# Kernel tuning notes

Hardware: AMD Instinct MI355X
Metric: run time of the kernel (lower is better)

## Reference

```python
import jax, jax.numpy as jnp
import numpy as np

B, S, D, H, DFF, L = 16, 1024, 64, 4, 256, 2
DEPTH = D // H
C1, C2, NOUT = 64, 64, 1
EPS = 1e-6


def setup_inputs() -> dict:
    key = jax.random.key(0)
    ks = jax.random.split(key, 24)
    s = 0.02
    vals = jax.random.normal(ks[0], (B, S), jnp.float32)
    nanp = jax.random.uniform(ks[1], (B, S)) < 0.1
    inputs = jnp.where(nanp, jnp.nan, vals)
    inp = {
        'inputs': inputs,
        'embedding': jax.random.normal(ks[2], (S, D - 1), jnp.float32) * s,
        'wq': jax.random.normal(ks[3], (L, D, D), jnp.float32) * s,
        'wq_b': jnp.zeros((L, D), jnp.float32),
        'wk': jax.random.normal(ks[4], (L, D, D), jnp.float32) * s,
        'wk_b': jnp.zeros((L, D), jnp.float32),
        'wv': jax.random.normal(ks[5], (L, D, D), jnp.float32) * s,
        'wv_b': jnp.zeros((L, D), jnp.float32),
        'wo': jax.random.normal(ks[6], (L, D, D), jnp.float32) * s,
        'ffn_w1': jax.random.normal(ks[7], (L, D, DFF), jnp.float32) * s,
        'ffn_w2': jax.random.normal(ks[8], (L, DFF, D), jnp.float32) * s,
        'ln1_g': jnp.ones((L, D), jnp.float32),
        'ln1_b': jnp.zeros((L, D), jnp.float32),
        'ln2_g': jnp.ones((L, D), jnp.float32),
        'ln2_b': jnp.zeros((L, D), jnp.float32),
        'c_w1': jax.random.normal(ks[9], (D, C1), jnp.float32) * s,
        'c_b1': jnp.zeros((C1,), jnp.float32),
        'c_w2': jax.random.normal(ks[10], (C1, C2), jnp.float32) * s,
        'c_b2': jnp.zeros((C2,), jnp.float32),
        'c_w3': jax.random.normal(ks[11], (C2, NOUT), jnp.float32) * s,
        'c_b3': jnp.zeros((NOUT,), jnp.float32),
        'out_bias': jax.random.normal(ks[12], (1, NOUT), jnp.float32),
    }
    return inp


def _layer_norm(x, g, b):
    m = jnp.mean(x, axis=-1, keepdims=True)
    v = jnp.mean((x - m) ** 2, axis=-1, keepdims=True)
    return (x - m) / jnp.sqrt(v + EPS) * g + b


def _forward(inputs, embedding, wq, wq_b, wk, wk_b, wv, wv_b, wo,
             ffn_w1, ffn_w2, ln1_g, ln1_b, ln2_g, ln2_b,
             c_w1, c_b1, c_w2, c_b2, c_w3, c_b3, out_bias):
    nan_mask = jnp.isnan(inputs)                           # (B,S) bool
    x_in = jnp.where(nan_mask, jnp.zeros_like(inputs), inputs)
    # mask (B,1,S,S): masked if either attribute i or j is NaN
    mask = (nan_mask[:, :, None] | nan_mask[:, None, :]).astype(jnp.float32)[:, None, :, :]
    # keep factor: zeros out NaN attribute rows after each sub-block  (B,S,1)
    keep = 1.0 - jnp.transpose(jnp.prod(mask, axis=-1), (0, 2, 1))

    # positional/attribute embedding: table * sqrt(d-1) * sqrt(d)
    attr = embedding * jnp.sqrt(jnp.float32(D - 1)) * jnp.sqrt(jnp.float32(D))  # (S, D-1)
    attr = jnp.broadcast_to(attr[None], (B, S, D - 1))
    x = jnp.concatenate([attr, x_in[:, :, None]], axis=2)  # (B,S,D)
    x = x * keep

    scale = 1.0 / jnp.sqrt(jnp.float32(DEPTH))
    for i in range(L):
        q = (x @ wq[i] + wq_b[i]).reshape(B, S, H, DEPTH).transpose(0, 2, 1, 3)
        k = (x @ wk[i] + wk_b[i]).reshape(B, S, H, DEPTH).transpose(0, 2, 1, 3)
        v = (x @ wv[i] + wv_b[i]).reshape(B, S, H, DEPTH).transpose(0, 2, 1, 3)
        logits = jnp.einsum('bhqd,bhkd->bhqk', q, k) * scale + mask * (-1e9)
        attn = jax.nn.softmax(logits, axis=-1) * (1.0 - mask)  # post-softmax multiplicative mask
        ctx = jnp.einsum('bhqk,bhkd->bhqd', attn, v)
        ctx = ctx.transpose(0, 2, 1, 3).reshape(B, S, D) @ wo[i]
        out1 = _layer_norm(x + ctx, ln1_g[i], ln1_b[i]) * keep
        ffn = jax.nn.relu(out1 @ ffn_w1[i]) @ ffn_w2[i]
        x = _layer_norm(out1 + ffn, ln2_g[i], ln2_b[i]) * keep

    h = jax.nn.relu(x @ c_w1 + c_b1)
    h = jax.nn.relu(h @ c_w2 + c_b2)
    phi = h @ c_w3 + c_b3                                   # (B,S,NOUT)
    y = jnp.sum(phi, axis=1) + out_bias                     # (B,NOUT)
    return y


def reference(inputs, embedding, wq, wq_b, wk, wk_b, wv, wv_b, wo,
              ffn_w1, ffn_w2, ln1_g, ln1_b, ln2_g, ln2_b,
              c_w1, c_b1, c_w2, c_b2, c_w3, c_b3, out_bias):
    return _forward(inputs, embedding, wq, wq_b, wk, wk_b, wv, wv_b, wo,
                    ffn_w1, ffn_w2, ln1_g, ln1_b, ln2_g, ln2_b,
                    c_w1, c_b1, c_w2, c_b2, c_w3, c_b3, out_bias)
```

## Files before the change

### kernel.cpp

```cpp
#include <hip/hip_runtime.h>
#include <hip/hip_bf16.h>
#include <math.h>

#define BB 16
#define SS 1024
#define DD 64
#define HH 4
#define DEPTH 16
#define DFF 256
#define NROWS (BB*SS)
#define EPSV 1e-6f
#define NKSPLIT 8
#define KCHUNK (SS / NKSPLIT)

__device__ __forceinline__ float bcast(float x, int kk) {
  return __int_as_float(__builtin_amdgcn_readlane(__float_as_int(x), kk));
}

__global__ __launch_bounds__(256) void build_x_kernel(
    const float* __restrict__ inputs, const float* __restrict__ emb,
    float* __restrict__ x, float* __restrict__ keep) {
  int gid = blockIdx.x * 256 + threadIdx.x;
  int row = gid >> 6;
  int d = gid & 63;
  int s = row & (SS - 1);
  float vin = inputs[row];
  bool nan = __builtin_isnan(vin);
  float kp = nan ? 0.0f : 1.0f;
  if (d == 0) keep[row] = kp;
  float val;
  if (d < 63) {
    const float scale = 7.93725393319377f * 8.0f;
    val = emb[s * 63 + d] * scale;
  } else {
    val = nan ? 0.0f : vin;
  }
  x[row * 64 + d] = val * kp;
}

__global__ __launch_bounds__(64, 2) void qkv_kernel(
    const float* __restrict__ xin,
    const float* __restrict__ wq, const float* __restrict__ wqb,
    const float* __restrict__ wk, const float* __restrict__ wkb,
    const float* __restrict__ wv, const float* __restrict__ wvb,
    float* __restrict__ q, float* __restrict__ k, float* __restrict__ v) {
  int lane = threadIdx.x;
  float wqc[64], wkc[64], wvc[64];
#pragma unroll
  for (int kk = 0; kk < 64; ++kk) {
    wqc[kk] = wq[kk * 64 + lane];
    wkc[kk] = wk[kk * 64 + lane];
    wvc[kk] = wv[kk * 64 + lane];
  }
  float bq = wqb[lane], bk = wkb[lane], bv = wvb[lane];
  int h = lane >> 4, dep = lane & 15;
  int row0 = blockIdx.x * 8;
  for (int r = row0; r < row0 + 8; ++r) {
    float xr = xin[r * 64 + lane];
    float qa0 = 0.f, qa1 = 0.f, ka0 = 0.f, ka1 = 0.f, va0 = 0.f, va1 = 0.f;
#pragma unroll
    for (int kk = 0; kk < 64; kk += 2) {
      float x0 = bcast(xr, kk);
      float x1 = bcast(xr, kk + 1);
      qa0 = fmaf(x0, wqc[kk], qa0); qa1 = fmaf(x1, wqc[kk + 1], qa1);
      ka0 = fmaf(x0, wkc[kk], ka0); ka1 = fmaf(x1, wkc[kk + 1], ka1);
      va0 = fmaf(x0, wvc[kk], va0); va1 = fmaf(x1, wvc[kk + 1], va1);
    }
    int b = r >> 10, s = r & (SS - 1);
    size_t o = (size_t)(((b * HH + h) * SS + s)) * DEPTH + dep;
    q[o] = qa0 + qa1 + bq;
    k[o] = ka0 + ka1 + bk;
    v[o] = va0 + va1 + bv;
  }
}

__global__ __launch_bounds__(256, 4) void attn_partial_kernel(
    const float* __restrict__ q, const float* __restrict__ k,
    const float* __restrict__ v, const float* __restrict__ keep,
    float* __restrict__ pA, float* __restrict__ pL) {
  __shared__ __align__(16) float klds[KCHUNK * DEPTH];
  __shared__ __align__(16) float vlds[KCHUNK * DEPTH];
  __shared__ float kplds[KCHUNK];
  int tid = threadIdx.x;
  int p = blockIdx.x * 256 + tid;
  int c = blockIdx.y;
  int bh = p >> 9;
  int s0 = p & 511;
  int b = bh >> 2;

  const float4* kbase = (const float4*)(k + ((size_t)bh * SS + c * KCHUNK) * DEPTH);
  const float4* vbase = (const float4*)(v + ((size_t)bh * SS + c * KCHUNK) * DEPTH);
#pragma unroll
  for (int i = 0; i < KCHUNK * 4 / 256; ++i) {
    ((float4*)klds)[tid + i * 256] = kbase[tid + i * 256];
    ((float4*)vlds)[tid + i * 256] = vbase[tid + i * 256];
  }
  if (tid < KCHUNK) kplds[tid] = keep[b * SS + c * KCHUNK + tid];
  __syncthreads();

  size_t rowA = (size_t)bh * SS + s0;
  size_t rowB = rowA + 512;
  const float4* qa4 = (const float4*)(q + rowA * DEPTH);
  const float4* qb4 = (const float4*)(q + rowB * DEPTH);
  float4 qA0 = qa4[0], qA1 = qa4[1], qA2 = qa4[2], qA3 = qa4[3];
  float4 qB0 = qb4[0], qB1 = qb4[1], qB2 = qb4[2], qB3 = qb4[3];
  float4 z = make_float4(0.f, 0.f, 0.f, 0.f);
  float4 aA0 = z, aA1 = z, aA2 = z, aA3 = z;
  float4 aB0 = z, aB1 = z, aB2 = z, aB3 = z;
  float lA = 0.0f, lB = 0.0f;
  for (int j = 0; j < KCHUNK; ++j) {
    float kpj = kplds[j];
    if (kpj == 0.0f) continue;
    const float4* kl = (const float4*)&klds[j * DEPTH];
    float4 k0 = kl[0], k1 = kl[1], k2 = kl[2], k3 = kl[3];
    const float4* vl = (const float4*)&vlds[j * DEPTH];
    float4 v0 = vl[0], v1 = vl[1], v2 = vl[2], v3 = vl[3];
    float dA0 = qA0.x * k0.x, dA1 = qA2.x * k2.x;
    float dB0 = qB0.x * k0.x, dB1 = qB2.x * k2.x;
    dA0 = fmaf(qA0.y, k0.y, dA0); dA1 = fmaf(qA2.y, k2.y, dA1);
    dB0 = fmaf(qB0.y, k0.y, dB0); dB1 = fmaf(qB2.y, k2.y, dB1);
    dA0 = fmaf(qA0.z, k0.z, dA0); dA1 = fmaf(qA2.z, k2.z, dA1);
    dB0 = fmaf(qB0.z, k0.z, dB0); dB1 = fmaf(qB2.z, k2.z, dB1);
    dA0 = fmaf(qA0.w, k0.w, dA0); dA1 = fmaf(qA2.w, k2.w, dA1);
    dB0 = fmaf(qB0.w, k0.w, dB0); dB1 = fmaf(qB2.w, k2.w, dB1);
    dA0 = fmaf(qA1.x, k1.x, dA0); dA1 = fmaf(qA3.x, k3.x, dA1);
    dB0 = fmaf(qB1.x, k1.x, dB0); dB1 = fmaf(qB3.x, k3.x, dB1);
    dA0 = fmaf(qA1.y, k1.y, dA0); dA1 = fmaf(qA3.y, k3.y, dA1);
    dB0 = fmaf(qB1.y, k1.y, dB0); dB1 = fmaf(qB3.y, k3.y, dB1);
    dA0 = fmaf(qA1.z, k1.z, dA0); dA1 = fmaf(qA3.z, k3.z, dA1);
    dB0 = fmaf(qB1.z, k1.z, dB0); dB1 = fmaf(qB3.z, k3.z, dB1);
    dA0 = fmaf(qA1.w, k1.w, dA0); dA1 = fmaf(qA3.w, k3.w, dA1);
    dB0 = fmaf(qB1.w, k1.w, dB0); dB1 = fmaf(qB3.w, k3.w, dB1);
    float pa = __expf((dA0 + dA1) * 0.25f) * kpj;
    float pb = __expf((dB0 + dB1) * 0.25f) * kpj;
    lA += pa; lB += pb;
    aA0.x = fmaf(pa, v0.x, aA0.x); aB0.x = fmaf(pb, v0.x, aB0.x);
    aA0.y = fmaf(pa, v0.y, aA0.y); aB0.y = fmaf(pb, v0.y, aB0.y);
    aA0.z = fmaf(pa, v0.z, aA0.z); aB0.z = fmaf(pb, v0.z, aB0.z);
    aA0.w = fmaf(pa, v0.w, aA0.w); aB0.w = fmaf(pb, v0.w, aB0.w);
    aA1.x = fmaf(pa, v1.x, aA1.x); aB1.x = fmaf(pb, v1.x, aB1.x);
    aA1.y = fmaf(pa, v1.y, aA1.y); aB1.y = fmaf(pb, v1.y, aB1.y);
    aA1.z = fmaf(pa, v1.z, aA1.z); aB1.z = fmaf(pb, v1.z, aB1.z);
    aA1.w = fmaf(pa, v1.w, aA1.w); aB1.w = fmaf(pb, v1.w, aB1.w);
    aA2.x = fmaf(pa, v2.x, aA2.x); aB2.x = fmaf(pb, v2.x, aB2.x);
    aA2.y = fmaf(pa, v2.y, aA2.y); aB2.y = fmaf(pb, v2.y, aB2.y);
    aA2.z = fmaf(pa, v2.z, aA2.z); aB2.z = fmaf(pb, v2.z, aB2.z);
    aA2.w = fmaf(pa, v2.w, aA2.w); aB2.w = fmaf(pb, v2.w, aB2.w);
    aA3.x = fmaf(pa, v3.x, aA3.x); aB3.x = fmaf(pb, v3.x, aB3.x);
    aA3.y = fmaf(pa, v3.y, aA3.y); aB3.y = fmaf(pb, v3.y, aB3.y);
    aA3.z = fmaf(pa, v3.z, aA3.z); aB3.z = fmaf(pb, v3.z, aB3.z);
    aA3.w = fmaf(pa, v3.w, aA3.w); aB3.w = fmaf(pb, v3.w, aB3.w);
  }
  size_t oA = ((size_t)c << 16) + rowA;
  size_t oB = ((size_t)c << 16) + rowB;
  pL[oA] = lA; pL[oB] = lB;
  float4* o4a = (float4*)(pA + oA * 16);
  o4a[0] = aA0; o4a[1] = aA1; o4a[2] = aA2; o4a[3] = aA3;
  float4* o4b = (float4*)(pA + oB * 16);
  o4b[0] = aB0; o4b[1] = aB1; o4b[2] = aB2; o4b[3] = aB3;
}

__global__ __launch_bounds__(256) void wo_ln1_kernel(
    const float* __restrict__ pA, const float* __restrict__ pL,
    const float* __restrict__ xin,
    const float* __restrict__ wo, const float* __restrict__ g,
    const float* __restrict__ bta, const float* __restrict__ keep,
    float* __restrict__ out1) {
  int tid = threadIdx.x;
  int lane = tid & 63;
  float woc[64];
#pragma unroll
  for (int kk = 0; kk < 64; ++kk) woc[kk] = wo[kk * 64 + lane];
  float gg = g[lane], bb = bta[lane];
  int wave = tid >> 6;
  int row0 = blockIdx.x * 16 + wave * 4;
  for (int r = row0; r < row0 + 4; ++r) {
    int b = r >> 10, s = r & (SS - 1);
    int h = lane >> 4, dep = lane & 15;
    size_t rowi = ((size_t)(b * HH + h) << 10) + s;
    float num = 0.0f, den = 0.0f;
#pragma unroll
    for (int c = 0; c < NKSPLIT; ++c) {
      num += pA[(((size_t)c << 16) + rowi) * 16 + dep];
      den += pL[((size_t)c << 16) + rowi];
    }
    float cr = num * keep[r] / den;
    float a0 = 0.f, a1 = 0.f;
#pragma unroll
    for (int kk = 0; kk < 64; kk += 2) {
      a0 = fmaf(bcast(cr, kk), woc[kk], a0);
      a1 = fmaf(bcast(cr, kk + 1), woc[kk + 1], a1);
    }
    float t = a0 + a1 + xin[r * 64 + lane];
    float sum = t;
#pragma unroll
    for (int off = 32; off; off >>= 1) sum += __shfl_xor(sum, off, 64);
    float mean = sum * (1.0f / 64.0f);
    float dv = t - mean;
    float sq = dv * dv;
#pragma unroll
    for (int off = 32; off; off >>= 1) sq += __shfl_xor(sq, off, 64);
    float var = sq * (1.0f / 64.0f);
    float o = dv * rsqrtf(var + EPSV) * gg + bb;
    out1[r * 64 + lane] = o * keep[r];
  }
}

__global__ __launch_bounds__(256) void ffn_fused_kernel(
    const float* __restrict__ out1, const float* __restrict__ w1,
    const float* __restrict__ w2, const float* __restrict__ g,
    const float* __restrict__ bta, const float* __restrict__ keep,
    float* __restrict__ xout) {
  __shared__ float part[4][4][64];
  int tid = threadIdx.x, wave = tid >> 6, lane = tid & 63;
  float w1c[64], w2c[64];
#pragma unroll
  for (int kk = 0; kk < 64; ++kk)
    w1c[kk] = w1[kk * 256 + wave * 64 + lane];
#pragma unroll
  for (int j = 0; j < 64; ++j)
    w2c[j] = w2[(wave * 64 + j) * 64 + lane];
  float gg = g[lane], bb = bta[lane];
  int row0 = blockIdx.x * 16;
  for (int grp = 0; grp < 4; ++grp) {
    int rbase = row0 + grp * 4;
    float xr0 = out1[(rbase + 0) * 64 + lane];
    float xr1 = out1[(rbase + 1) * 64 + lane];
    float xr2 = out1[(rbase + 2) * 64 + lane];
    float xr3 = out1[(rbase + 3) * 64 + lane];
    float xrs[4] = {xr0, xr1, xr2, xr3};
#pragma unroll
    for (int r = 0; r < 4; ++r) {
      float h0 = 0.f, h1 = 0.f;
#pragma unroll
      for (int kk = 0; kk < 64; kk += 2) {
        h0 = fmaf(bcast(xrs[r], kk), w1c[kk], h0);
        h1 = fmaf(bcast(xrs[r], kk + 1), w1c[kk + 1], h1);
      }
      float hv = fmaxf(h0 + h1, 0.0f);
      float y0 = 0.f, y1 = 0.f;
#pragma unroll
      for (int j = 0; j < 64; j += 2) {
        y0 = fmaf(bcast(hv, j), w2c[j], y0);
        y1 = fmaf(bcast(hv, j + 1), w2c[j + 1], y1);
      }
      part[r][wave][lane] = y0 + y1;
    }
    __syncthreads();
    float xres = (wave == 0) ? xr0 : (wave == 1) ? xr1 : (wave == 2) ? xr2 : xr3;
    float t = part[wave][0][lane] + part[wave][1][lane] +
              part[wave][2][lane] + part[wave][3][lane] + xres;
    float sum = t;
#pragma unroll
    for (int off = 32; off; off >>= 1) sum += __shfl_xor(sum, off, 64);
    float mean = sum * (1.0f / 64.0f);
    float dv = t - mean;
    float sq = dv * dv;
#pragma unroll
    for (int off = 32; off; off >>= 1) sq += __shfl_xor(sq, off, 64);
    float var = sq * (1.0f / 64.0f);
    float o = dv * rsqrtf(var + EPSV) * gg + bb;
    xout[(rbase + wave) * 64 + lane] = o * keep[rbase + wave];
    __syncthreads();
  }
}

__global__ void init_out_kernel(const float* __restrict__ out_bias,
                                float* __restrict__ out) {
  if (threadIdx.x < BB) out[threadIdx.x] = out_bias[0];
}

__global__ __launch_bounds__(256, 3) void classifier_kernel(
    const float* __restrict__ x,
    const float* __restrict__ w1, const float* __restrict__ b1,
    const float* __restrict__ w2, const float* __restrict__ b2,
    const float* __restrict__ w3, const float* __restrict__ b3,
    float* __restrict__ out) {
  int tid = threadIdx.x;
  int lane = tid & 63, wave = tid >> 6;
  float w1c[64], w2c[64];
#pragma unroll
  for (int kk = 0; kk < 64; ++kk) {
    w1c[kk] = w1[kk * 64 + lane];
    w2c[kk] = w2[kk * 64 + lane];
  }
  float w3d = w3[lane];
  float bb1 = b1[lane], bb2 = b2[lane], b3v = b3[0];
  int row0 = blockIdx.x * 32 + wave * 8;
  float wavesum = 0.0f;
  for (int r = row0; r < row0 + 8; ++r) {
    float xr = x[r * 64 + lane];
    float h1a = 0.f, h1b = 0.f;
#pragma unroll
    for (int kk = 0; kk < 64; kk += 2) {
      h1a = fmaf(bcast(xr, kk), w1c[kk], h1a);
      h1b = fmaf(bcast(xr, kk + 1), w1c[kk + 1], h1b);
    }
    float h1 = fmaxf(h1a + h1b + bb1, 0.0f);
    float h2a = 0.f, h2b = 0.f;
#pragma unroll
    for (int kk = 0; kk < 64; kk += 2) {
      h2a = fmaf(bcast(h1, kk), w2c[kk], h2a);
      h2b = fmaf(bcast(h1, kk + 1), w2c[kk + 1], h2b);
    }
    float h2 = fmaxf(h2a + h2b + bb2, 0.0f);
    float p = h2 * w3d;
#pragma unroll
    for (int off = 32; off; off >>= 1) p += __shfl_xor(p, off, 64);
    wavesum += p + b3v;
  }
  if (lane == 0) {
    int b = row0 >> 10;
    atomicAdd(&out[b], wavesum);
  }
}

extern "C" void kernel_launch(void* const* d_in, const int* in_sizes, int n_in,
                              void* d_out, int out_size, void* d_ws, size_t ws_size,
                              hipStream_t stream) {
  const float* inputs = (const float*)d_in[0];
  const float* emb    = (const float*)d_in[1];
  const float* wq     = (const float*)d_in[2];
  const float* wqb    = (const float*)d_in[3];
  const float* wk     = (const float*)d_in[4];
  const float* wkb    = (const float*)d_in[5];
  const float* wv     = (const float*)d_in[6];
  const float* wvb    = (const float*)d_in[7];
  const float* wo     = (const float*)d_in[8];
  const float* fw1    = (const float*)d_in[9];
  const float* fw2    = (const float*)d_in[10];
  const float* l1g    = (const float*)d_in[11];
  const float* l1b    = (const float*)d_in[12];
  const float* l2g    = (const float*)d_in[13];
  const float* l2b    = (const float*)d_in[14];
  const float* cw1    = (const float*)d_in[15];
  const float* cb1    = (const float*)d_in[16];
  const float* cw2    = (const float*)d_in[17];
  const float* cb2    = (const float*)d_in[18];
  const float* cw3    = (const float*)d_in[19];
  const float* cb3    = (const float*)d_in[20];
  const float* obias  = (const float*)d_in[21];
  float* out = (float*)d_out;

  float* ws   = (float*)d_ws;
  float* x    = ws;
  float* keep = x    + (size_t)NROWS * 64;
  float* q    = keep + NROWS;
  float* k    = q    + (size_t)NROWS * 64;
  float* v    = k    + (size_t)NROWS * 64;
  float* out1 = v    + (size_t)NROWS * 64;
  float* pA   = out1 + (size_t)NROWS * 64;
  float* pL   = pA   + (size_t)NKSPLIT * 65536 * 16;

  build_x_kernel<<<4096, 256, 0, stream>>>(inputs, emb, x, keep);

  for (int i = 0; i < 2; ++i) {
    qkv_kernel<<<2048, 64, 0, stream>>>(
        x, wq + i * 4096, wqb + i * 64, wk + i * 4096, wkb + i * 64,
        wv + i * 4096, wvb + i * 64, q, k, v);
    attn_partial_kernel<<<dim3(128, NKSPLIT), 256, 0, stream>>>(
        q, k, v, keep, pA, pL);
    wo_ln1_kernel<<<1024, 256, 0, stream>>>(
        pA, pL, x, wo + i * 4096, l1g + i * 64, l1b + i * 64, keep, out1);
    ffn_fused_kernel<<<1024, 256, 0, stream>>>(
        out1, fw1 + i * 16384, fw2 + i * 16384, l2g + i * 64, l2b + i * 64,
        keep, x);
  }

  init_out_kernel<<<1, 64, 0, stream>>>(obias, out);
  classifier_kernel<<<512, 256, 0, stream>>>(x, cw1, cb1, cw2, cb2, cw3, cb3, out);
}
```

Before: 397.8 us.

## Split QKV projection across three waves and software-pipeline K loads in attention

```diff
diff --git a/kernel.cpp b/kernel.cpp
--- a/kernel.cpp
+++ b/kernel.cpp
@@ -38,39 +38,36 @@
   x[row * 64 + d] = val * kp;
 }
 
-__global__ __launch_bounds__(64, 2) void qkv_kernel(
+__global__ __launch_bounds__(192, 4) void qkv_kernel(
     const float* __restrict__ xin,
     const float* __restrict__ wq, const float* __restrict__ wqb,
     const float* __restrict__ wk, const float* __restrict__ wkb,
     const float* __restrict__ wv, const float* __restrict__ wvb,
     float* __restrict__ q, float* __restrict__ k, float* __restrict__ v) {
-  int lane = threadIdx.x;
-  float wqc[64], wkc[64], wvc[64];
-#pragma unroll
-  for (int kk = 0; kk < 64; ++kk) {
-    wqc[kk] = wq[kk * 64 + lane];
-    wkc[kk] = wk[kk * 64 + lane];
-    wvc[kk] = wv[kk * 64 + lane];
-  }
-  float bq = wqb[lane], bk = wkb[lane], bv = wvb[lane];
+  int tid = threadIdx.x;
+  int wave = tid >> 6, lane = tid & 63;
+  const float* wsel = (wave == 0) ? wq : (wave == 1) ? wk : wv;
+  const float* bsel = (wave == 0) ? wqb : (wave == 1) ? wkb : wvb;
+  float* outp = (wave == 0) ? q : (wave == 1) ? k : v;
+  float wc[64];
+#pragma unroll
+  for (int kk = 0; kk < 64; ++kk) wc[kk] = wsel[kk * 64 + lane];
+  float bias = bsel[lane];
   int h = lane >> 4, dep = lane & 15;
   int row0 = blockIdx.x * 8;
   for (int r = row0; r < row0 + 8; ++r) {
     float xr = xin[r * 64 + lane];
-    float qa0 = 0.f, qa1 = 0.f, ka0 = 0.f, ka1 = 0.f, va0 = 0.f, va1 = 0.f;
-#pragma unroll
-    for (int kk = 0; kk < 64; kk += 2) {
-      float x0 = bcast(xr, kk);
-      float x1 = bcast(xr, kk + 1);
-      qa0 = fmaf(x0, wqc[kk], qa0); qa1 = fmaf(x1, wqc[kk + 1], qa1);
-      ka0 = fmaf(x0, wkc[kk], ka0); ka1 = fmaf(x1, wkc[kk + 1], ka1);
-      va0 = fmaf(x0, wvc[kk], va0); va1 = fmaf(x1, wvc[kk + 1], va1);
+    float a0 = 0.f, a1 = 0.f, a2 = 0.f, a3 = 0.f;
+#pragma unroll
+    for (int kk = 0; kk < 64; kk += 4) {
+      a0 = fmaf(bcast(xr, kk + 0), wc[kk + 0], a0);
+      a1 = fmaf(bcast(xr, kk + 1), wc[kk + 1], a1);
+      a2 = fmaf(bcast(xr, kk + 2), wc[kk + 2], a2);
+      a3 = fmaf(bcast(xr, kk + 3), wc[kk + 3], a3);
     }
     int b = r >> 10, s = r & (SS - 1);
     size_t o = (size_t)(((b * HH + h) * SS + s)) * DEPTH + dep;
-    q[o] = qa0 + qa1 + bq;
-    k[o] = ka0 + ka1 + bk;
-    v[o] = va0 + va1 + bv;
+    outp[o] = (a0 + a1) + (a2 + a3) + bias;
   }
 }
 
@@ -78,7 +75,7 @@
     const float* __restrict__ q, const float* __restrict__ k,
     const float* __restrict__ v, const float* __restrict__ keep,
     float* __restrict__ pA, float* __restrict__ pL) {
-  __shared__ __align__(16) float klds[KCHUNK * DEPTH];
+  __shared__ __align__(16) float klds[(KCHUNK + 1) * DEPTH];
   __shared__ __align__(16) float vlds[KCHUNK * DEPTH];
   __shared__ float kplds[KCHUNK];
   int tid = threadIdx.x;
@@ -108,13 +105,15 @@
   float4 aA0 = z, aA1 = z, aA2 = z, aA3 = z;
   float4 aB0 = z, aB1 = z, aB2 = z, aB3 = z;
   float lA = 0.0f, lB = 0.0f;
+  const float4* kl4 = (const float4*)klds;
+  const float4* vl4 = (const float4*)vlds;
+  float4 k0 = kl4[0], k1 = kl4[1], k2 = kl4[2], k3 = kl4[3];
   for (int j = 0; j < KCHUNK; ++j) {
+    float4 nk0 = kl4[(j + 1) * 4 + 0], nk1 = kl4[(j + 1) * 4 + 1];
+    float4 nk2 = kl4[(j + 1) * 4 + 2], nk3 = kl4[(j + 1) * 4 + 3];
+    float4 v0 = vl4[j * 4 + 0], v1 = vl4[j * 4 + 1];
+    float4 v2 = vl4[j * 4 + 2], v3 = vl4[j * 4 + 3];
     float kpj = kplds[j];
-    if (kpj == 0.0f) continue;
-    const float4* kl = (const float4*)&klds[j * DEPTH];
-    float4 k0 = kl[0], k1 = kl[1], k2 = kl[2], k3 = kl[3];
-    const float4* vl = (const float4*)&vlds[j * DEPTH];
-    float4 v0 = vl[0], v1 = vl[1], v2 = vl[2], v3 = vl[3];
     float dA0 = qA0.x * k0.x, dA1 = qA2.x * k2.x;
     float dB0 = qB0.x * k0.x, dB1 = qB2.x * k2.x;
     dA0 = fmaf(qA0.y, k0.y, dA0); dA1 = fmaf(qA2.y, k2.y, dA1);
@@ -150,6 +149,7 @@
     aA3.y = fmaf(pa, v3.y, aA3.y); aB3.y = fmaf(pb, v3.y, aB3.y);
     aA3.z = fmaf(pa, v3.z, aA3.z); aB3.z = fmaf(pb, v3.z, aB3.z);
     aA3.w = fmaf(pa, v3.w, aA3.w); aB3.w = fmaf(pb, v3.w, aB3.w);
+    k0 = nk0; k1 = nk1; k2 = nk2; k3 = nk3;
   }
   size_t oA = ((size_t)c << 16) + rowA;
   size_t oB = ((size_t)c << 16) + rowB;
@@ -355,7 +355,7 @@
   build_x_kernel<<<4096, 256, 0, stream>>>(inputs, emb, x, keep);
 
   for (int i = 0; i < 2; ++i) {
-    qkv_kernel<<<2048, 64, 0, stream>>>(
+    qkv_kernel<<<2048, 192, 0, stream>>>(
         x, wq + i * 4096, wqb + i * 64, wk + i * 4096, wkb + i * 64,
         wv + i * 4096, wvb + i * 64, q, k, v);
     attn_partial_kernel<<<dim3(128, NKSPLIT), 256, 0, stream>>>(
```

Result: no change. 404.4 us (+1.7%).
